# Performance work log

Hardware: AMD Instinct MI355X
Metric: run time of the kernel (lower is better)

The kernel has to match this reference:

```python
import jax, jax.numpy as jnp
import numpy as np

CROP_H = 14
CROP_W = 14
EXTRAPOLATION_VALUE = 0.0


def _crop_and_resize(image, boxes, box_ind, crop_h, crop_w, extrapolation_value):
    # image: [B, C, H, W], boxes: [N, 4] normalized (y1, x1, y2, x2), box_ind: [N]
    B, C, H, W = image.shape
    y1, x1, y2, x2 = boxes[:, 0], boxes[:, 1], boxes[:, 2], boxes[:, 3]

    # TF crop_and_resize coordinate mapping (crop_h, crop_w > 1 case)
    height_scale = (y2 - y1) * (H - 1) / (crop_h - 1)  # [N]
    width_scale = (x2 - x1) * (W - 1) / (crop_w - 1)   # [N]
    iy = jnp.arange(crop_h, dtype=image.dtype)
    ix = jnp.arange(crop_w, dtype=image.dtype)
    in_y = y1[:, None] * (H - 1) + iy[None, :] * height_scale[:, None]  # [N, crop_h]
    in_x = x1[:, None] * (W - 1) + ix[None, :] * width_scale[:, None]   # [N, crop_w]

    valid_y = (in_y >= 0) & (in_y <= H - 1)  # [N, crop_h]
    valid_x = (in_x >= 0) & (in_x <= W - 1)  # [N, crop_w]

    top = jnp.floor(in_y)
    left = jnp.floor(in_x)
    ly = (in_y - top)[:, :, None, None]   # [N, crop_h, 1, 1]
    lx = (in_x - left)[:, None, :, None]  # [N, 1, crop_w, 1]

    top_i = jnp.clip(top.astype(jnp.int32), 0, H - 1)          # [N, crop_h]
    bot_i = jnp.clip(top_i + 1, 0, H - 1)
    left_i = jnp.clip(left.astype(jnp.int32), 0, W - 1)        # [N, crop_w]
    right_i = jnp.clip(left_i + 1, 0, W - 1)

    b = box_ind[:, None, None]            # [N, 1, 1]
    yt = top_i[:, :, None]                # [N, crop_h, 1]
    yb = bot_i[:, :, None]
    xl = left_i[:, None, :]               # [N, 1, crop_w]
    xr = right_i[:, None, :]

    # advanced indexing -> [N, crop_h, crop_w, C]
    tl = image[b, :, yt, xl]
    tr = image[b, :, yt, xr]
    bl = image[b, :, yb, xl]
    br = image[b, :, yb, xr]

    top_v = tl + (tr - tl) * lx
    bot_v = bl + (br - bl) * lx
    val = top_v + (bot_v - top_v) * ly    # [N, crop_h, crop_w, C]

    mask = (valid_y[:, :, None] & valid_x[:, None, :])[:, :, :, None]
    val = jnp.where(mask, val, jnp.asarray(extrapolation_value, image.dtype))
    return jnp.transpose(val, (0, 3, 1, 2))  # [N, C, crop_h, crop_w]


def setup_inputs() -> dict:
    key = jax.random.key(0)
    k1, k2, k3 = jax.random.split(key, 3)
    B, C, H, W = 8, 256, 200, 200
    N = 1000
    image = jax.random.normal(k1, (B, C, H, W), dtype=jnp.float32)
    boxes = jax.random.uniform(k2, (N, 4), dtype=jnp.float32)
    box_ind = jax.random.randint(k3, (N,), 0, B, dtype=jnp.int32)
    return {"image": image, "boxes": boxes, "box_ind": box_ind}


def reference(image, boxes, box_ind):
    return _crop_and_resize(image, boxes, box_ind, CROP_H, CROP_W, EXTRAPOLATION_VALUE)
```

## Files before the change

### kernel.cpp

```cpp
#include <hip/hip_runtime.h>


#define CROP_H 14
#define CROP_W 14
#define CROP_HW (CROP_H * CROP_W)
#define C_DIM 256
#define H_DIM 200
#define W_DIM 200
#define HW (H_DIM * W_DIM)
#define PER_BOX (C_DIM * CROP_HW)
#define BLOCK 256
#define CHUNKS 4
#define C_PER (C_DIM / CHUNKS)
#define ELEMS (C_PER * CROP_HW)
#define ITERS (ELEMS / BLOCK)
#define NXCD 8

__global__ __launch_bounds__(BLOCK) void sort_boxes_kernel(
    const int* __restrict__ box_ind, int N, int* __restrict__ perm)
{
    __shared__ int cnt[8];
    __shared__ int base[8];
    const int t = threadIdx.x;
    if (t < 8) cnt[t] = 0;
    __syncthreads();
    for (int i = t; i < N; i += BLOCK) atomicAdd(&cnt[box_ind[i]], 1);
    __syncthreads();
    if (t == 0) {
        int run = 0;
        for (int b = 0; b < 8; ++b) { base[b] = run; run += cnt[b]; }
    }
    __syncthreads();
    for (int i = t; i < N; i += BLOCK) {
        const int pos = atomicAdd(&base[box_ind[i]], 1);
        perm[pos] = i;
    }
}

__global__ __launch_bounds__(BLOCK, 6) void crop_and_resize_kernel(
    const float* __restrict__ image,
    const float* __restrict__ boxes,
    const int*   __restrict__ box_ind,
    const int*   __restrict__ perm,
    float*       __restrict__ out,
    int N)
{
    __shared__ int4   s_d[CROP_HW];
    __shared__ float2 s_w[CROP_HW];
    __shared__ int s_n, s_b;

    const int nwg = gridDim.x;
    int wgid = blockIdx.x;
    if ((nwg % NXCD) == 0) {
        const int per = nwg / NXCD;
        wgid = (wgid % NXCD) * per + wgid / NXCD;
    }
    const int chunk = wgid / N;
    const int slot  = wgid - chunk * N;
    const int t     = threadIdx.x;

    if (t == 0) {
        const int n = perm[slot];
        s_n = n;
        s_b = box_ind[n];
    }
    __syncthreads();
    const int n = s_n;

    if (t < CROP_HW) {
        const int iy = t / CROP_W;
        const int ix = t - iy * CROP_W;
        const float y1 = boxes[n * 4 + 0];
        const float x1 = boxes[n * 4 + 1];
        const float y2 = boxes[n * 4 + 2];
        const float x2 = boxes[n * 4 + 3];

        const float hs   = (y2 - y1) * (float)(H_DIM - 1) / (float)(CROP_H - 1);
        const float ws   = (x2 - x1) * (float)(W_DIM - 1) / (float)(CROP_W - 1);
        const float in_y = y1 * (float)(H_DIM - 1) + (float)iy * hs;
        const float in_x = x1 * (float)(W_DIM - 1) + (float)ix * ws;

        const int vy = (in_y >= 0.0f) && (in_y <= (float)(H_DIM - 1));
        const int vx = (in_x >= 0.0f) && (in_x <= (float)(W_DIM - 1));

        const float top  = floorf(in_y);
        const float left = floorf(in_x);
        const float ly   = in_y - top;
        const float lx   = in_x - left;

        int ti = (int)top;
        ti = min(max(ti, 0), H_DIM - 1);
        const int bi = min(ti + 1, H_DIM - 1);
        int li = (int)left;
        li = min(max(li, 0), W_DIM - 1);
        const int ri = min(li + 1, W_DIM - 1);

        s_d[t] = make_int4(ti * W_DIM + li, ri - li, (bi - ti) * W_DIM, vy & vx);
        s_w[t] = make_float2(ly, lx);
    }
    __syncthreads();

    const float* __restrict__ imgb = image + (size_t)s_b * (C_DIM * HW)
                                           + (size_t)chunk * (C_PER * HW);
    float* __restrict__ outb = out + (size_t)n * PER_BOX + (size_t)chunk * ELEMS;

    #pragma unroll 7
    for (int k = 0; k < ITERS; ++k) {
        const int j = t + k * BLOCK;
        const int c = j / CROP_HW;
        const int p = j - c * CROP_HW;

        const int4   d = s_d[p];
        const float2 w = s_w[p];

        const float* __restrict__ basec = imgb + (size_t)c * HW + d.x;
        const float tl = basec[0];
        const float tr = basec[d.y];
        const float bl = basec[d.z];
        const float br = basec[d.z + d.y];

        const float top_v = fmaf(tr - tl, w.y, tl);
        const float bot_v = fmaf(br - bl, w.y, bl);
        float v = fmaf(bot_v - top_v, w.x, top_v);
        v = d.w ? v : 0.0f;
        outb[j] = v;
    }
}

extern "C" void kernel_launch(void* const* d_in, const int* in_sizes, int n_in,
                              void* d_out, int out_size, void* d_ws, size_t ws_size,
                              hipStream_t stream) {
    const float* image   = (const float*)d_in[0];
    const float* boxes   = (const float*)d_in[1];
    const int*   box_ind = (const int*)d_in[2];
    float*       out     = (float*)d_out;
    int*         perm    = (int*)d_ws;

    const int N = in_sizes[2];

    sort_boxes_kernel<<<dim3(1), dim3(BLOCK), 0, stream>>>(box_ind, N, perm);
    crop_and_resize_kernel<<<dim3(N * CHUNKS), dim3(BLOCK), 0, stream>>>(
        image, boxes, box_ind, perm, out, N);
}
```

Before: 708.3 us.

## Stage box row spans into LDS per channel before bilinear interpolation

For each channel, the kernel now cooperatively loads the 28 source rows covering the box's x-span into a shared-memory tile, using coalesced loads and magic-number division. It then interpolates all 196 crop points from LDS. Per-box y/x parameters are computed separately, and validity is applied as a multiplicative mask. The aim is to replace scattered global gathers with contiguous row reads. The cost is two barriers per channel, serialized channel processing with less memory-level parallelism, and extra bytes read for wide boxes. Occupancy is also hinted up to 7 blocks.

```diff
diff --git a/kernel.cpp b/kernel.cpp
--- a/kernel.cpp
+++ b/kernel.cpp
@@ -12,8 +12,8 @@
 #define BLOCK 256
 #define CHUNKS 4
 #define C_PER (C_DIM / CHUNKS)
-#define ELEMS (C_PER * CROP_HW)
-#define ITERS (ELEMS / BLOCK)
+#define NSLOT (2 * CROP_H)
+#define MAXW 201
 #define NXCD 8
 
 __global__ __launch_bounds__(BLOCK) void sort_boxes_kernel(
@@ -37,7 +37,7 @@
     }
 }
 
-__global__ __launch_bounds__(BLOCK, 6) void crop_and_resize_kernel(
+__global__ __launch_bounds__(BLOCK, 7) void crop_and_resize_kernel(
     const float* __restrict__ image,
     const float* __restrict__ boxes,
     const int*   __restrict__ box_ind,
@@ -45,9 +45,13 @@
     float*       __restrict__ out,
     int N)
 {
-    __shared__ int4   s_d[CROP_HW];
-    __shared__ float2 s_w[CROP_HW];
-    __shared__ int s_n, s_b;
+    __shared__ float s_tile[NSLOT * MAXW];
+    __shared__ int   s_rowoff[NSLOT];
+    __shared__ int   s_li[CROP_W], s_dr[CROP_W];
+    __shared__ float s_ly[CROP_H], s_lx[CROP_W];
+    __shared__ float s_vy[CROP_H], s_vx[CROP_W];
+    __shared__ int   s_n, s_b, s_minli, s_span, s_sw;
+    __shared__ unsigned s_magic;
 
     const int nwg = gridDim.x;
     int wgid = blockIdx.x;
@@ -59,71 +63,119 @@
     const int slot  = wgid - chunk * N;
     const int t     = threadIdx.x;
 
-    if (t == 0) {
-        const int n = perm[slot];
-        s_n = n;
-        s_b = box_ind[n];
-    }
+    if (t == 0) { const int nn = perm[slot]; s_n = nn; s_b = box_ind[nn]; }
     __syncthreads();
     const int n = s_n;
 
-    if (t < CROP_HW) {
-        const int iy = t / CROP_W;
-        const int ix = t - iy * CROP_W;
+    if (t < CROP_H + CROP_W) {
         const float y1 = boxes[n * 4 + 0];
         const float x1 = boxes[n * 4 + 1];
         const float y2 = boxes[n * 4 + 2];
         const float x2 = boxes[n * 4 + 3];
-
-        const float hs   = (y2 - y1) * (float)(H_DIM - 1) / (float)(CROP_H - 1);
-        const float ws   = (x2 - x1) * (float)(W_DIM - 1) / (float)(CROP_W - 1);
-        const float in_y = y1 * (float)(H_DIM - 1) + (float)iy * hs;
-        const float in_x = x1 * (float)(W_DIM - 1) + (float)ix * ws;
-
-        const int vy = (in_y >= 0.0f) && (in_y <= (float)(H_DIM - 1));
-        const int vx = (in_x >= 0.0f) && (in_x <= (float)(W_DIM - 1));
-
-        const float top  = floorf(in_y);
-        const float left = floorf(in_x);
-        const float ly   = in_y - top;
-        const float lx   = in_x - left;
-
-        int ti = (int)top;
-        ti = min(max(ti, 0), H_DIM - 1);
-        const int bi = min(ti + 1, H_DIM - 1);
-        int li = (int)left;
-        li = min(max(li, 0), W_DIM - 1);
-        const int ri = min(li + 1, W_DIM - 1);
-
-        s_d[t] = make_int4(ti * W_DIM + li, ri - li, (bi - ti) * W_DIM, vy & vx);
-        s_w[t] = make_float2(ly, lx);
+        if (t < CROP_H) {
+            const float hs   = (y2 - y1) * (float)(H_DIM - 1) / (float)(CROP_H - 1);
+            const float in_y = y1 * (float)(H_DIM - 1) + (float)t * hs;
+            const float top  = floorf(in_y);
+            int ti = (int)top;
+            ti = min(max(ti, 0), H_DIM - 1);
+            const int bi = min(ti + 1, H_DIM - 1);
+            s_rowoff[2 * t]     = ti * W_DIM;
+            s_rowoff[2 * t + 1] = bi * W_DIM;
+            s_ly[t] = in_y - top;
+            s_vy[t] = (in_y >= 0.0f && in_y <= (float)(H_DIM - 1)) ? 1.0f : 0.0f;
+        } else {
+            const int ix = t - CROP_H;
+            const float ws   = (x2 - x1) * (float)(W_DIM - 1) / (float)(CROP_W - 1);
+            const float in_x = x1 * (float)(W_DIM - 1) + (float)ix * ws;
+            const float left = floorf(in_x);
+            int li = (int)left;
+            li = min(max(li, 0), W_DIM - 1);
+            const int ri = min(li + 1, W_DIM - 1);
+            s_li[ix] = li;
+            s_dr[ix] = ri - li;
+            s_lx[ix] = in_x - left;
+            s_vx[ix] = (in_x >= 0.0f && in_x <= (float)(W_DIM - 1)) ? 1.0f : 0.0f;
+        }
     }
     __syncthreads();
 
-    const float* __restrict__ imgb = image + (size_t)s_b * (C_DIM * HW)
-                                           + (size_t)chunk * (C_PER * HW);
-    float* __restrict__ outb = out + (size_t)n * PER_BOX + (size_t)chunk * ELEMS;
+    if (t == 0) {
+        int mn = W_DIM, mx = 0;
+        for (int i = 0; i < CROP_W; ++i) {
+            mn = min(mn, s_li[i]);
+            mx = max(mx, s_li[i] + s_dr[i]);
+        }
+        const int span = mx - mn + 1;
+        s_minli = mn;
+        s_span  = span;
+        s_sw    = span | 1;
+        s_magic = (unsigned)(0x100000000ULL / (unsigned)span) + 1u;
+    }
+    __syncthreads();
+    const int minli = s_minli;
+    if (t < NSLOT) s_rowoff[t] += minli;
+    __syncthreads();
 
-    #pragma unroll 7
-    for (int k = 0; k < ITERS; ++k) {
-        const int j = t + k * BLOCK;
-        const int c = j / CROP_HW;
-        const int p = j - c * CROP_HW;
+    const int span = s_span;
+    const int sw   = s_sw;
+    const unsigned magic = s_magic;
+    const int T    = NSLOT * span;
+    const int Tm1  = T - 1;
 
-        const int4   d = s_d[p];
-        const float2 w = s_w[p];
+    const float* __restrict__ imgc =
+        image + ((size_t)s_b * C_DIM + (size_t)(chunk * C_PER)) * HW;
+    float* __restrict__ outp =
+        out + (size_t)n * PER_BOX + (size_t)(chunk * C_PER) * CROP_HW + t;
 
-        const float* __restrict__ basec = imgb + (size_t)c * HW + d.x;
-        const float tl = basec[0];
-        const float tr = basec[d.y];
-        const float bl = basec[d.z];
-        const float br = basec[d.z + d.y];
+    const bool act = (t < CROP_HW);
+    int topoff = 0, dr = 0;
+    float ly = 0.0f, lx = 0.0f, vf = 0.0f;
+    if (act) {
+        const int iy = t / CROP_W;
+        const int ix = t - iy * CROP_W;
+        topoff = (2 * iy) * sw + (s_li[ix] - minli);
+        dr = s_dr[ix];
+        ly = s_ly[iy];
+        lx = s_lx[ix];
+        vf = s_vy[iy] * s_vx[ix];
+    }
 
-        const float top_v = fmaf(tr - tl, w.y, tl);
-        const float bot_v = fmaf(br - bl, w.y, bl);
-        float v = fmaf(bot_v - top_v, w.x, top_v);
-        v = d.w ? v : 0.0f;
-        outb[j] = v;
+    for (int c = 0; c < C_PER; ++c) {
+        const float* __restrict__ imgch = imgc + (size_t)c * HW;
+
+        for (int i0 = t; i0 < T; i0 += 4 * BLOCK) {
+            const int i1 = min(i0 + 1 * BLOCK, Tm1);
+            const int i2 = min(i0 + 2 * BLOCK, Tm1);
+            const int i3 = min(i0 + 3 * BLOCK, Tm1);
+            const int sa = (int)__umulhi((unsigned)i0, magic);
+            const int sb = (int)__umulhi((unsigned)i1, magic);
+            const int sc = (int)__umulhi((unsigned)i2, magic);
+            const int sd = (int)__umulhi((unsigned)i3, magic);
+            const int xa = i0 - sa * span;
+            const int xb = i1 - sb * span;
+            const int xc = i2 - sc * span;
+            const int xd = i3 - sd * span;
+            const float va = imgch[s_rowoff[sa] + xa];
+            const float vb = imgch[s_rowoff[sb] + xb];
+            const float vc = imgch[s_rowoff[sc] + xc];
+            const float vd = imgch[s_rowoff[sd] + xd];
+            s_tile[sa * sw + xa] = va;
+            s_tile[sb * sw + xb] = vb;
+            s_tile[sc * sw + xc] = vc;
+            s_tile[sd * sw + xd] = vd;
+        }
+        __syncthreads();
+
+        if (act) {
+            const float tl = s_tile[topoff];
+            const float tr = s_tile[topoff + dr];
+            const float bl = s_tile[topoff + sw];
+            const float br = s_tile[topoff + sw + dr];
+            const float tv = fmaf(tr - tl, lx, tl);
+            const float bv = fmaf(br - bl, lx, bl);
+            outp[c * CROP_HW] = fmaf(bv - tv, ly, tv) * vf;
+        }
+        __syncthreads();
     }
 }
 
```

New measurement: 828.6 us. 1.17x slower.
